# Kernel tuning notes

Measured on AMD Instinct MI355X. Metric: run time of the kernel, lower is better.

The kernel has to match this reference:

```python
import jax, jax.numpy as jnp
import numpy as np

D_MODEL = 768
NUM_HEADS = 12
NUM_REG = 4
EPS = 1e-5


def _layernorm(x, g, b):
    mu = jnp.mean(x, axis=-1, keepdims=True)
    var = jnp.mean(jnp.square(x - mu), axis=-1, keepdims=True)
    return (x - mu) * jax.lax.rsqrt(var + EPS) * g + b


def _make_mask(seq_len):
    # True = masked (disallowed), matching torch attn_mask bool semantics.
    r1 = 1 + NUM_REG
    mask = np.ones((seq_len, seq_len), dtype=bool)
    mask[0, :] = False                      # context token attends to all
    mask[1:r1, :] = False                   # register tokens attend to all
    mask[r1:, :r1] = False                  # (not use_input_context_token) == False
    mask[r1:, r1:] = ~np.eye(seq_len - r1, dtype=bool)  # feature tokens: self only
    return jnp.asarray(mask)


def setup_inputs() -> dict:
    key = jax.random.key(0)
    ks = jax.random.split(key, 16)
    B, C, H, W = 8, D_MODEL, 32, 32
    d = D_MODEL
    s = 0.02
    inp = {
        "x": jax.random.normal(ks[0], (B, C, H, W), jnp.float32),
        "context_token": jax.random.normal(ks[1], (B, 1, d), jnp.float32),
        "register_tokens": jax.random.normal(ks[2], (B, NUM_REG, d), jnp.float32),
        "in_proj_w": jax.random.normal(ks[3], (3 * d, d), jnp.float32) * s,
        "in_proj_b": jnp.zeros((3 * d,), jnp.float32),
        "out_w": jax.random.normal(ks[4], (d, d), jnp.float32) * s,
        "out_b": jnp.zeros((d,), jnp.float32),
        "ln1_g": jnp.ones((d,), jnp.float32),
        "ln1_b": jnp.zeros((d,), jnp.float32),
        "ln2_g": jnp.ones((d,), jnp.float32),
        "ln2_b": jnp.zeros((d,), jnp.float32),
        "w1": jax.random.normal(ks[5], (4 * d, d), jnp.float32) * s,
        "b1": jnp.zeros((4 * d,), jnp.float32),
        "w2": jax.random.normal(ks[6], (d, 4 * d), jnp.float32) * s,
        "b2": jnp.zeros((d,), jnp.float32),
    }
    return inp


def reference(x, context_token, register_tokens, in_proj_w, in_proj_b,
              out_w, out_b, ln1_g, ln1_b, ln2_g, ln2_b, w1, b1, w2, b2):
    B, C, H, W = x.shape
    d, nh = D_MODEL, NUM_HEADS
    hd = d // nh
    x_flat = x.reshape(B, C, H * W).transpose(0, 2, 1)          # [B, HW, d]
    tokens = jnp.concatenate([context_token, register_tokens], axis=1)
    xw = _layernorm(jnp.concatenate([tokens, x_flat], axis=1), ln1_g, ln1_b)  # [B, S, d]
    S = xw.shape[1]

    qkv = xw @ in_proj_w.T + in_proj_b                           # [B, S, 3d]
    q, k, v = jnp.split(qkv, 3, axis=-1)
    q = q.reshape(B, S, nh, hd).transpose(0, 2, 1, 3)            # [B, nh, S, hd]
    k = k.reshape(B, S, nh, hd).transpose(0, 2, 1, 3)
    v = v.reshape(B, S, nh, hd).transpose(0, 2, 1, 3)

    scores = jnp.einsum("bhqd,bhkd->bhqk", q, k) / jnp.sqrt(jnp.float32(hd))
    mask = _make_mask(S)
    scores = jnp.where(mask, jnp.float32(-1e9), scores)
    probs = jax.nn.softmax(scores, axis=-1)
    attn = jnp.einsum("bhqk,bhkd->bhqd", probs, v)               # [B, nh, S, hd]
    attn = attn.transpose(0, 2, 1, 3).reshape(B, S, d)
    attn = attn @ out_w.T + out_b

    h1 = attn + xw                                                # residual
    ff = _layernorm(h1, ln2_g, ln2_b)
    ff = jax.nn.gelu(ff @ w1.T + b1, approximate=False) @ w2.T + b2
    out = ff + h1                                                 # [B, S, d]

    r1 = 1 + NUM_REG
    ctx_out = out[:, 0:1, :]
    reg_out = out[:, 1:r1, :]
    feat_out = out[:, r1:, :].transpose(0, 2, 1).reshape(B, C, H, W)
    return feat_out, ctx_out, reg_out
```

## Files before the change

kernel.cpp:

```cpp
#include <hip/hip_runtime.h>
#include <math.h>
#include <stdint.h>

#define SEQ 1029
#define BATCH 8
#define M_TOT (BATCH * SEQ)
#define M_PAD 8320
#define NCHUNK 17

typedef float floatx4 __attribute__((ext_vector_type(4)));
typedef __bf16 bf16x8 __attribute__((ext_vector_type(8)));

__device__ __forceinline__ unsigned short f2bf(float f) {
  union { float f; unsigned u; } v; v.f = f;
  unsigned r = v.u + 0x7fffu + ((v.u >> 16) & 1u);
  return (unsigned short)(r >> 16);
}
__device__ __forceinline__ float bf2f(unsigned short h) {
  union { unsigned u; float f; } v; v.u = ((unsigned)h) << 16;
  return v.f;
}
__device__ __forceinline__ float bf_lo(unsigned u) { union { unsigned x; float f; } v; v.x = u << 16; return v.f; }
__device__ __forceinline__ float bf_hi(unsigned u) { union { unsigned x; float f; } v; v.x = u & 0xffff0000u; return v.f; }

__device__ __forceinline__ float wave_sum(float v) {
#pragma unroll
  for (int off = 32; off > 0; off >>= 1) v += __shfl_xor(v, off, 64);
  return v;
}
__device__ __forceinline__ float wave_max(float v) {
#pragma unroll
  for (int off = 32; off > 0; off >>= 1) v = fmaxf(v, __shfl_xor(v, off, 64));
  return v;
}

__device__ __forceinline__ void gload16(const unsigned short* g, unsigned short* l) {
  __builtin_amdgcn_global_load_lds(
      (const __attribute__((address_space(1))) unsigned int*)g,
      (__attribute__((address_space(3))) unsigned int*)l, 16, 0, 0);
}

template <int C>
__device__ __forceinline__ void vwait() {
  if constexpr (C == 0) asm volatile("s_waitcnt vmcnt(0)" ::: "memory");
  else if constexpr (C == 4) asm volatile("s_waitcnt vmcnt(4)" ::: "memory");
  else asm volatile("s_waitcnt vmcnt(8)" ::: "memory");
}

#define NQ_QKV 442368
#define NQ_OUT 147456
#define NQ_W1  589824
#define NQ_W2  589824
#define NQ_PAD 8448
__global__ void convert_all(const float4* __restrict__ inw, const float4* __restrict__ outw,
                            const float4* __restrict__ w1, const float4* __restrict__ w2,
                            ushort4* __restrict__ wqkv, ushort4* __restrict__ wout,
                            ushort4* __restrict__ w1b, ushort4* __restrict__ w2b,
                            ushort4* __restrict__ xw_pad, ushort4* __restrict__ attn_pad) {
  const int i = blockIdx.x * 256 + threadIdx.x;
  const float4* src; ushort4* dst; int off;
  if (i < NQ_QKV) { src = inw; dst = wqkv; off = i; }
  else if (i < NQ_QKV + NQ_OUT) { src = outw; dst = wout; off = i - NQ_QKV; }
  else if (i < NQ_QKV + NQ_OUT + NQ_W1) { src = w1; dst = w1b; off = i - NQ_QKV - NQ_OUT; }
  else if (i < NQ_QKV + NQ_OUT + NQ_W1 + NQ_W2) { src = w2; dst = w2b; off = i - NQ_QKV - NQ_OUT - NQ_W1; }
  else {
    const int j = i - (NQ_QKV + NQ_OUT + NQ_W1 + NQ_W2);
    const ushort4 z = {0, 0, 0, 0};
    if (j < NQ_PAD) { xw_pad[j] = z; attn_pad[j] = z; }
    return;
  }
  const float4 v = src[off];
  ushort4 o;
  o.x = f2bf(v.x); o.y = f2bf(v.y); o.z = f2bf(v.z); o.w = f2bf(v.w);
  dst[off] = o;
}
#define NQ_ALL (NQ_QKV + NQ_OUT + NQ_W1 + NQ_W2 + NQ_PAD)

__global__ __launch_bounds__(256) void ln1_feat(const float* __restrict__ x,
                                                const float* __restrict__ g,
                                                const float* __restrict__ bta,
                                                unsigned short* __restrict__ xw) {
  __shared__ float tile[768 * 17];
  const int b = blockIdx.y;
  const int hw0 = blockIdx.x * 16;
  const int t = threadIdx.x;
  const float* xb = x + (size_t)b * 768 * 1024;
  const int cl = t >> 4, hl = t & 15;
  for (int it = 0; it < 48; it++) {
    const int c = it * 16 + cl;
    tile[c * 17 + hl] = xb[(size_t)c * 1024 + hw0 + hl];
  }
  __syncthreads();
  const int wave = t >> 6, lane = t & 63;
  for (int tk = wave; tk < 16; tk += 4) {
    float vals[12], s = 0.f, ss = 0.f;
#pragma unroll
    for (int i = 0; i < 12; i++) {
      const float v = tile[(lane + 64 * i) * 17 + tk];
      vals[i] = v; s += v; ss += v * v;
    }
    s = wave_sum(s); ss = wave_sum(ss);
    const float mu = s * (1.0f / 768.0f);
    const float var = ss * (1.0f / 768.0f) - mu * mu;
    const float rs = rsqrtf(var + 1e-5f);
    const int row = b * SEQ + 5 + hw0 + tk;
    unsigned short* orow = xw + (size_t)row * 768;
#pragma unroll
    for (int i = 0; i < 12; i++) {
      const int c = lane + 64 * i;
      orow[c] = f2bf((vals[i] - mu) * rs * g[c] + bta[c]);
    }
  }
}

__global__ __launch_bounds__(256) void ln1_special(const float* __restrict__ ctx,
                                                   const float* __restrict__ regs,
                                                   const float* __restrict__ g,
                                                   const float* __restrict__ bta,
                                                   unsigned short* __restrict__ xw) {
  const int gw = blockIdx.x * 4 + (threadIdx.x >> 6);
  const int lane = threadIdx.x & 63;
  if (gw >= 40) return;
  const int b = gw / 5, s = gw % 5;
  const float* src = (s == 0) ? (ctx + (size_t)b * 768)
                              : (regs + ((size_t)b * 4 + (s - 1)) * 768);
  float vals[12], sm = 0.f, ss = 0.f;
#pragma unroll
  for (int i = 0; i < 12; i++) {
    const float v = src[lane + 64 * i];
    vals[i] = v; sm += v; ss += v * v;
  }
  sm = wave_sum(sm); ss = wave_sum(ss);
  const float mu = sm * (1.0f / 768.0f);
  const float var = ss * (1.0f / 768.0f) - mu * mu;
  const float rs = rsqrtf(var + 1e-5f);
  unsigned short* orow = xw + (size_t)(b * SEQ + s) * 768;
#pragma unroll
  for (int i = 0; i < 12; i++) {
    const int c = lane + 64 * i;
    orow[c] = f2bf((vals[i] - mu) * rs * g[c] + bta[c]);
  }
}

#define BM 128
#define BN 128
#define BK 32

template <int EPI, int K, int N, int NBUF>
__global__ __launch_bounds__(256, NBUF == 3 ? 3 : 2) void gemm_bt(
    const unsigned short* __restrict__ A,
    const unsigned short* __restrict__ W,
    const float* __restrict__ bias,
    const unsigned short* __restrict__ residb,
    const float* __restrict__ residf,
    float* __restrict__ outf,
    unsigned short* __restrict__ outb) {
  __shared__ alignas(16) unsigned short As[NBUF][BM * BK];
  __shared__ alignas(16) unsigned short Ws[NBUF][BN * BK];
  const int t = threadIdx.x;
  const int wave = t >> 6, lane = t & 63;
  const int quad = lane >> 4, l16 = lane & 15;
  const int wm = (wave & 1) * 64, wn = (wave >> 1) * 64;

  constexpr int GX = N / BN;
  constexpr int NWG = GX * (M_PAD / BM);
  constexpr int Q8 = NWG / 8, R8 = NWG % 8;
  const int flat = blockIdx.y * GX + blockIdx.x;
  const int xcd = flat & 7, idx = flat >> 3;
  const int wgid = (xcd < R8 ? xcd * (Q8 + 1) : R8 * (Q8 + 1) + (xcd - R8) * Q8) + idx;
  const int tileM = (wgid / GX) * BM;
  const int tileN = (wgid % GX) * BN;

  const int rl = lane >> 2;
  const int kc8 = ((lane & 3) ^ ((rl >> 1) & 3)) * 8;
  const unsigned short* Ag = A + (size_t)(tileM + wave * 16 + rl) * K;
  const unsigned short* Wg = W + (size_t)(tileN + wave * 16 + rl) * K;
  const int ldst = wave * 512 + lane * 8;

  const int koff = ((quad ^ ((l16 >> 1) & 3)) * 8);

  const floatx4 zero4 = {0.f, 0.f, 0.f, 0.f};
  floatx4 acc[4][4];
#pragma unroll
  for (int i = 0; i < 4; i++)
#pragma unroll
    for (int j = 0; j < 4; j++) acc[i][j] = zero4;

  auto dma = [&](int k0, int buf) {
    gload16(Ag + k0 + kc8, &As[buf][0] + ldst);
    gload16(Ag + (size_t)64 * K + k0 + kc8, &As[buf][0] + ldst + 2048);
    gload16(Wg + k0 + kc8, &Ws[buf][0] + ldst);
    gload16(Wg + (size_t)64 * K + k0 + kc8, &Ws[buf][0] + ldst + 2048);
  };
  auto compute = [&](int buf) {
    bf16x8 af[4], wf[4];
#pragma unroll
    for (int i = 0; i < 4; i++)
      af[i] = *(const bf16x8*)(&As[buf][0] + (wm + i * 16 + l16) * BK + koff);
#pragma unroll
    for (int j = 0; j < 4; j++)
      wf[j] = *(const bf16x8*)(&Ws[buf][0] + (wn + j * 16 + l16) * BK + koff);
#pragma unroll
    for (int i = 0; i < 4; i++)
#pragma unroll
      for (int j = 0; j < 4; j++)
        acc[i][j] = __builtin_amdgcn_mfma_f32_16x16x32_bf16(af[i], wf[j], acc[i][j], 0, 0, 0);
  };

  constexpr int NSTEP = K / BK;
  constexpr int PF = NBUF - 1;

#pragma unroll
  for (int p = 0; p < PF; ++p) dma(p * BK, p);

  int cb = 0, db = PF % NBUF;
#pragma unroll 1
  for (int i = 0; i < NSTEP - PF; ++i) {
    vwait<4 * (NBUF - 2)>();
    __builtin_amdgcn_s_barrier();
    __builtin_amdgcn_sched_barrier(0);
    dma((i + PF) * BK, db);
    db = (db + 1 == NBUF) ? 0 : db + 1;
    compute(cb);
    cb = (cb + 1 == NBUF) ? 0 : cb + 1;
  }
  if constexpr (NBUF == 4) {
    vwait<8>(); __builtin_amdgcn_s_barrier(); __builtin_amdgcn_sched_barrier(0);
    compute(cb); cb = (cb + 1 == NBUF) ? 0 : cb + 1;
  }
  vwait<4>(); __builtin_amdgcn_s_barrier(); __builtin_amdgcn_sched_barrier(0);
  compute(cb); cb = (cb + 1 == NBUF) ? 0 : cb + 1;
  vwait<0>(); __builtin_amdgcn_s_barrier(); __builtin_amdgcn_sched_barrier(0);
  compute(cb);

#pragma unroll
  for (int i = 0; i < 4; i++) {
    const int mbase = tileM + wm + i * 16 + quad * 4;
#pragma unroll
    for (int j = 0; j < 4; j++) {
      const int n = tileN + wn + j * 16 + l16;
      const float bv = bias[n];
#pragma unroll
      for (int r = 0; r < 4; r++) {
        const size_t idx2 = (size_t)(mbase + r) * N + n;
        float v = acc[i][j][r] + bv;
        if constexpr (EPI == 0) {
          outb[idx2] = f2bf(v);
        } else if constexpr (EPI == 1) {
          outf[idx2] = v + bf2f(residb[idx2]);
        } else if constexpr (EPI == 2) {
          v = 0.5f * v * (1.0f + erff(v * 0.70710678118654752f));
          outb[idx2] = f2bf(v);
        } else {
          outf[idx2] = v + residf[idx2];
        }
      }
    }
  }
}

__global__ __launch_bounds__(256) void attn_feat(const unsigned short* __restrict__ qkv,
                                                 unsigned short* __restrict__ attn) {
  __shared__ float kk[5][64];
  __shared__ float vv[5][64];
  const int b = blockIdx.z, h = blockIdx.y;
  const int t = threadIdx.x;
  const size_t base = (size_t)b * SEQ;
  for (int i = t; i < 320; i += 256) {
    const int j = i >> 6, dd = i & 63;
    const size_t rb = (base + j) * 2304 + (size_t)h * 64 + dd;
    kk[j][dd] = bf2f(qkv[rb + 768]);
    vv[j][dd] = bf2f(qkv[rb + 1536]);
  }
  __syncthreads();
  const int wave = t >> 6, lane = t & 63;
  const int s = 5 + blockIdx.x * 4 + wave;
  const size_t row = (base + s) * 2304 + (size_t)h * 64;
  const float q = bf2f(qkv[row + lane]);
  const float kself = bf2f(qkv[row + 768 + lane]);
  const float vself = bf2f(qkv[row + 1536 + lane]);
  float sc[6];
#pragma unroll
  for (int j = 0; j < 5; j++) sc[j] = wave_sum(q * kk[j][lane]) * 0.125f;
  sc[5] = wave_sum(q * kself) * 0.125f;
  float mx = sc[0];
#pragma unroll
  for (int j = 1; j < 6; j++) mx = fmaxf(mx, sc[j]);
  float den = 0.f, e[6];
#pragma unroll
  for (int j = 0; j < 6; j++) { e[j] = expf(sc[j] - mx); den += e[j]; }
  const float inv = 1.0f / den;
  float o = 0.f;
#pragma unroll
  for (int j = 0; j < 5; j++) o += e[j] * vv[j][lane];
  o += e[5] * vself;
  attn[(base + s) * 768 + (size_t)h * 64 + lane] = f2bf(o * inv);
}

__global__ __launch_bounds__(256) void attn_part(const unsigned short* __restrict__ qkv,
                                                 float* __restrict__ part) {
  __shared__ float qs[5][64];
  __shared__ float sc[5][64];
  __shared__ float mArr[5], lArr[5];
  __shared__ float og[4][320];
  const int c = blockIdx.x, h = blockIdx.y, b = blockIdx.z;
  const int t = threadIdx.x;
  const size_t base = (size_t)b * SEQ;
  const int kbase = (c < 16) ? (5 + 64 * c) : 0;
  const int nvalid = (c < 16) ? 64 : 5;

  for (int i = t; i < 320; i += 256)
    qs[i >> 6][i & 63] = bf2f(qkv[(base + (i >> 6)) * 2304 + (size_t)h * 64 + (i & 63)]);
  __syncthreads();

  const int keyloc = t >> 2, dc = t & 3;
  const int key = kbase + keyloc;
  const unsigned short* krow = qkv + (base + key) * 2304 + 768 + (size_t)h * 64;
  const uint4 k0 = *(const uint4*)(krow + dc * 8);
  const uint4 k1 = *(const uint4*)(krow + dc * 8 + 32);
  float kf[16];
  {
    const unsigned ku[8] = {k0.x, k0.y, k0.z, k0.w, k1.x, k1.y, k1.z, k1.w};
#pragma unroll
    for (int j = 0; j < 8; j++) { kf[2 * j] = bf_lo(ku[j]); kf[2 * j + 1] = bf_hi(ku[j]); }
  }
#pragma unroll
  for (int q = 0; q < 5; q++) {
    const float* qp = qs[q];
    float d0 = 0.f;
#pragma unroll
    for (int j = 0; j < 8; j++) d0 += qp[dc * 8 + j] * kf[j];
#pragma unroll
    for (int j = 0; j < 8; j++) d0 += qp[dc * 8 + 32 + j] * kf[8 + j];
    d0 += __shfl_xor(d0, 1, 64);
    d0 += __shfl_xor(d0, 2, 64);
    if (dc == 0) sc[q][keyloc] = (keyloc < nvalid) ? d0 * 0.125f : -1e30f;
  }
  __syncthreads();

  const int wave = t >> 6, lane = t & 63;
  for (int q = wave; q < 5; q += 4) {
    const float v = sc[q][lane];
    const float m = wave_max(v);
    const float e = expf(v - m);
    sc[q][lane] = e;
    const float l = wave_sum(e);
    if (lane == 0) { mArr[q] = m; lArr[q] = l; }
  }
  __syncthreads();

  const int d = t & 63, g = t >> 6;
  float o[5] = {0.f, 0.f, 0.f, 0.f, 0.f};
  for (int i = 0; i < 16; i++) {
    const int kl = g * 16 + i;
    const float v = bf2f(qkv[(base + kbase + kl) * 2304 + 1536 + (size_t)h * 64 + d]);
#pragma unroll
    for (int q = 0; q < 5; q++) o[q] += sc[q][kl] * v;
  }
#pragma unroll
  for (int q = 0; q < 5; q++) og[g][q * 64 + d] = o[q];
  __syncthreads();

  float* pw = part + (size_t)((b * 12 + h) * NCHUNK + c) * 5 * 66;
  for (int i = t; i < 320; i += 256) {
    const int q = i >> 6, dd = i & 63;
    pw[q * 66 + 2 + dd] = og[0][i] + og[1][i] + og[2][i] + og[3][i];
    if (dd == 0) { pw[q * 66] = mArr[q]; pw[q * 66 + 1] = lArr[q]; }
  }
}

__global__ __launch_bounds__(64) void attn_comb(const float* __restrict__ part,
                                                unsigned short* __restrict__ attn) {
  const int qi = blockIdx.x, h = blockIdx.y, b = blockIdx.z;
  const int d = threadIdx.x;
  float M = -3e38f, L = 0.f, o = 0.f;
  for (int c = 0; c < NCHUNK; c++) {
    const float* p = part + ((size_t)((b * 12 + h) * NCHUNK + c) * 5 + qi) * 66;
    const float mc = p[0], lc = p[1], oc = p[2 + d];
    if (mc > M) {
      const float s = expf(M - mc);
      L = L * s + lc; o = o * s + oc; M = mc;
    } else {
      const float w = expf(mc - M);
      L += lc * w; o += oc * w;
    }
  }
  attn[((size_t)b * SEQ + qi) * 768 + (size_t)h * 64 + d] = f2bf(o / L);
}

__global__ __launch_bounds__(256) void ln2_kernel(const float* __restrict__ h1,
                                                  const float* __restrict__ g,
                                                  const float* __restrict__ bta,
                                                  unsigned short* __restrict__ out) {
  const int row = blockIdx.x * 4 + (threadIdx.x >> 6);
  const int lane = threadIdx.x & 63;
  const float* r = h1 + (size_t)row * 768;
  float vals[12], sm = 0.f, ss = 0.f;
#pragma unroll
  for (int i = 0; i < 12; i++) {
    const float v = r[lane + 64 * i];
    vals[i] = v; sm += v; ss += v * v;
  }
  sm = wave_sum(sm); ss = wave_sum(ss);
  const float mu = sm * (1.0f / 768.0f);
  const float var = ss * (1.0f / 768.0f) - mu * mu;
  const float rs = rsqrtf(var + 1e-5f);
  unsigned short* orow = out + (size_t)row * 768;
#pragma unroll
  for (int i = 0; i < 12; i++) {
    const int c = lane + 64 * i;
    orow[c] = f2bf((vals[i] - mu) * rs * g[c] + bta[c]);
  }
}

__global__ __launch_bounds__(256) void scatter_all(const float* __restrict__ outb,
                                                   float* __restrict__ dout) {
  const int t = threadIdx.x;
  const int b = blockIdx.z;
  if (blockIdx.x == 24) {
    const int i = (b * 32 + blockIdx.y) * 256 + t;
    if (i >= 40 * 768) return;
    const int rowi = i / 768, c = i % 768;
    const int bb = rowi / 5, s = rowi % 5;
    const float v = outb[(size_t)(bb * SEQ + s) * 768 + c];
    if (s == 0) dout[6291456 + (size_t)bb * 768 + c] = v;
    else dout[6291456 + 6144 + ((size_t)bb * 4 + (s - 1)) * 768 + c] = v;
    return;
  }
  __shared__ float tl[32][33];
  const int hw0 = blockIdx.y * 32, c0 = blockIdx.x * 32;
  const int i = t >> 5, j = t & 31;
#pragma unroll
  for (int r = 0; r < 4; r++) {
    const int hwi = i + r * 8;
    tl[hwi][j] = outb[(size_t)(b * SEQ + 5 + hw0 + hwi) * 768 + c0 + j];
  }
  __syncthreads();
#pragma unroll
  for (int r = 0; r < 4; r++) {
    const int ci = i + r * 8;
    dout[(size_t)b * 768 * 1024 + (size_t)(c0 + ci) * 1024 + hw0 + j] = tl[j][ci];
  }
}

extern "C" void kernel_launch(void* const* d_in, const int* in_sizes, int n_in,
                              void* d_out, int out_size, void* d_ws, size_t ws_size,
                              hipStream_t stream) {
  const float* x    = (const float*)d_in[0];
  const float* ctx  = (const float*)d_in[1];
  const float* regs = (const float*)d_in[2];
  const float* inw  = (const float*)d_in[3];
  const float* inb  = (const float*)d_in[4];
  const float* outw = (const float*)d_in[5];
  const float* outbi= (const float*)d_in[6];
  const float* ln1g = (const float*)d_in[7];
  const float* ln1b = (const float*)d_in[8];
  const float* ln2g = (const float*)d_in[9];
  const float* ln2b = (const float*)d_in[10];
  const float* w1   = (const float*)d_in[11];
  const float* b1   = (const float*)d_in[12];
  const float* w2   = (const float*)d_in[13];
  const float* b2   = (const float*)d_in[14];

  char* ws = (char*)d_ws;
  unsigned short* wqkv_b = (unsigned short*)(ws + 0);
  unsigned short* wout_b = (unsigned short*)(ws + 3538944);
  unsigned short* w1_b   = (unsigned short*)(ws + 4718592);
  unsigned short* w2_b   = (unsigned short*)(ws + 9437184);
  unsigned short* xw_b   = (unsigned short*)(ws + 14155776);
  unsigned short* ln2o_b = (unsigned short*)(ws + 26935296);
  float*          h1_f   = (float*)(ws + 39714816);
  unsigned short* qkv_b  = (unsigned short*)(ws + 65273856);
  unsigned short* attn_b = (unsigned short*)(ws + 103612416);
  float*          out_f  = (float*)(ws + 14155776);
  unsigned short* ffm_b  = (unsigned short*)(ws + 65273856);
  float*          part_f = (float*)(ws + 39714816);
  float* dout = (float*)d_out;

  convert_all<<<(NQ_ALL + 255) / 256, 256, 0, stream>>>(
      (const float4*)inw, (const float4*)outw, (const float4*)w1, (const float4*)w2,
      (ushort4*)wqkv_b, (ushort4*)wout_b, (ushort4*)w1_b, (ushort4*)w2_b,
      (ushort4*)(xw_b + (size_t)M_TOT * 768), (ushort4*)(attn_b + (size_t)M_TOT * 768));

  ln1_feat<<<dim3(64, 8), 256, 0, stream>>>(x, ln1g, ln1b, xw_b);
  ln1_special<<<10, 256, 0, stream>>>(ctx, regs, ln1g, ln1b, xw_b);

  gemm_bt<0, 768, 2304, 3><<<dim3(2304 / BN, M_PAD / BM), 256, 0, stream>>>(
      xw_b, wqkv_b, inb, nullptr, nullptr, nullptr, qkv_b);

  attn_feat<<<dim3(256, 12, 8), 256, 0, stream>>>(qkv_b, attn_b);
  attn_part<<<dim3(NCHUNK, 12, 8), 256, 0, stream>>>(qkv_b, part_f);
  attn_comb<<<dim3(5, 12, 8), 64, 0, stream>>>(part_f, attn_b);

  gemm_bt<1, 768, 768, 4><<<dim3(768 / BN, M_PAD / BM), 256, 0, stream>>>(
      attn_b, wout_b, outbi, xw_b, nullptr, h1_f, nullptr);

  ln2_kernel<<<M_PAD / 4, 256, 0, stream>>>(h1_f, ln2g, ln2b, ln2o_b);

  gemm_bt<2, 768, 3072, 3><<<dim3(3072 / BN, M_PAD / BM), 256, 0, stream>>>(
      ln2o_b, w1_b, b1, nullptr, nullptr, nullptr, ffm_b);

  gemm_bt<3, 3072, 768, 4><<<dim3(768 / BN, M_PAD / BM), 256, 0, stream>>>(
      ffm_b, w2_b, b2, nullptr, h1_f, out_f, nullptr);

  scatter_all<<<dim3(25, 32, 8), 256, 0, stream>>>(out_f, dout);
}
```

Baseline: 419.6 us.

## Add 256x256-tile XCD-swizzled GEMM for FFN1 and polynomial GELU

The FFN up-projection now uses a new 512-thread GEMM kernel with 256x256 tiles, a 4-buffer direct-to-LDS prefetch pipeline and an XCD-aware workgroup remap. The larger tile is meant to raise data reuse per LDS load and improve L2 locality for this large GEMM. Exact erff in the GELU epilogue is also replaced by an Abramowitz-Stegun polynomial using a fast reciprocal and exp. Risks: the M tiling does not divide M_PAD (8320/256), so the last tile row reads A past the padded rows, and the large LDS footprint limits occupancy.

```diff
diff --git a/kernel.cpp b/kernel.cpp
--- a/kernel.cpp
+++ b/kernel.cpp
@@ -32,6 +32,15 @@
 #pragma unroll
   for (int off = 32; off > 0; off >>= 1) v = fmaxf(v, __shfl_xor(v, off, 64));
   return v;
+}
+
+__device__ __forceinline__ float fast_gelu(float v) {
+  const float ax = fabsf(v) * 0.70710678118654752f;
+  const float t = __builtin_amdgcn_rcpf(1.0f + 0.3275911f * ax);
+  const float poly = ((((1.061405429f * t - 1.453152027f) * t + 1.421413741f) * t
+                       - 0.284496736f) * t + 0.254829592f) * t;
+  const float er = 1.0f - poly * __expf(-ax * ax);
+  return 0.5f * v * (1.0f + copysignf(er, v));
 }
 
 __device__ __forceinline__ void gload16(const unsigned short* g, unsigned short* l) {
@@ -249,10 +258,114 @@
         } else if constexpr (EPI == 1) {
           outf[idx2] = v + bf2f(residb[idx2]);
         } else if constexpr (EPI == 2) {
-          v = 0.5f * v * (1.0f + erff(v * 0.70710678118654752f));
-          outb[idx2] = f2bf(v);
+          outb[idx2] = f2bf(fast_gelu(v));
         } else {
           outf[idx2] = v + residf[idx2];
+        }
+      }
+    }
+  }
+}
+
+#define BM2 256
+#define BN2 256
+
+template <int EPI, int K, int N>
+__global__ __launch_bounds__(512, 2) void gemm_big(
+    const unsigned short* __restrict__ A,
+    const unsigned short* __restrict__ W,
+    const float* __restrict__ bias,
+    unsigned short* __restrict__ outb) {
+  __shared__ alignas(16) unsigned short As[4][BM2 * BK];
+  __shared__ alignas(16) unsigned short Ws[4][BN2 * BK];
+  const int t = threadIdx.x;
+  const int wave = t >> 6, lane = t & 63;
+  const int quad = lane >> 4, l16 = lane & 15;
+  const int wm = (wave & 1) * 128, wn = (wave >> 1) * 64;
+
+  constexpr int GX = N / BN2;
+  constexpr int GY = (M_PAD + BM2 - 1) / BM2;
+  constexpr int NWG = GX * GY;
+  constexpr int Q8 = NWG / 8, R8 = NWG % 8;
+  const int flat = blockIdx.y * GX + blockIdx.x;
+  const int xcd = flat & 7, idx = flat >> 3;
+  const int wgid = (xcd < R8 ? xcd * (Q8 + 1) : R8 * (Q8 + 1) + (xcd - R8) * Q8) + idx;
+  const int tileM = (wgid / GX) * BM2;
+  const int tileN = (wgid % GX) * BN2;
+
+  const int rl = lane >> 2;
+  const int kc8 = ((lane & 3) ^ ((rl >> 1) & 3)) * 8;
+  const unsigned short* Ag = A + (size_t)(tileM + wave * 16 + rl) * K;
+  const unsigned short* Wg = W + (size_t)(tileN + wave * 16 + rl) * K;
+  const int ldst = wave * 512 + lane * 8;
+
+  const int koff = ((quad ^ ((l16 >> 1) & 3)) * 8);
+
+  const floatx4 zero4 = {0.f, 0.f, 0.f, 0.f};
+  floatx4 acc[8][4];
+#pragma unroll
+  for (int i = 0; i < 8; i++)
+#pragma unroll
+    for (int j = 0; j < 4; j++) acc[i][j] = zero4;
+
+  auto dma = [&](int k0, int buf) {
+    gload16(Ag + k0 + kc8, &As[buf][0] + ldst);
+    gload16(Ag + (size_t)128 * K + k0 + kc8, &As[buf][0] + ldst + 4096);
+    gload16(Wg + k0 + kc8, &Ws[buf][0] + ldst);
+    gload16(Wg + (size_t)128 * K + k0 + kc8, &Ws[buf][0] + ldst + 4096);
+  };
+  auto compute = [&](int buf) {
+    bf16x8 af[8], wf[4];
+#pragma unroll
+    for (int i = 0; i < 8; i++)
+      af[i] = *(const bf16x8*)(&As[buf][0] + (wm + i * 16 + l16) * BK + koff);
+#pragma unroll
+    for (int j = 0; j < 4; j++)
+      wf[j] = *(const bf16x8*)(&Ws[buf][0] + (wn + j * 16 + l16) * BK + koff);
+#pragma unroll
+    for (int i = 0; i < 8; i++)
+#pragma unroll
+      for (int j = 0; j < 4; j++)
+        acc[i][j] = __builtin_amdgcn_mfma_f32_16x16x32_bf16(af[i], wf[j], acc[i][j], 0, 0, 0);
+  };
+
+  constexpr int NSTEP = K / BK;
+  constexpr int PF = 3;
+
+  dma(0, 0); dma(BK, 1); dma(2 * BK, 2);
+
+  int cb = 0, db = 3;
+#pragma unroll 1
+  for (int i = 0; i < NSTEP - PF; ++i) {
+    vwait<8>();
+    __builtin_amdgcn_s_barrier();
+    __builtin_amdgcn_sched_barrier(0);
+    dma((i + PF) * BK, db);
+    db = (db + 1) & 3;
+    compute(cb);
+    cb = (cb + 1) & 3;
+  }
+  vwait<8>(); __builtin_amdgcn_s_barrier(); __builtin_amdgcn_sched_barrier(0);
+  compute(cb); cb = (cb + 1) & 3;
+  vwait<4>(); __builtin_amdgcn_s_barrier(); __builtin_amdgcn_sched_barrier(0);
+  compute(cb); cb = (cb + 1) & 3;
+  vwait<0>(); __builtin_amdgcn_s_barrier(); __builtin_amdgcn_sched_barrier(0);
+  compute(cb);
+
+#pragma unroll
+  for (int i = 0; i < 8; i++) {
+    const int mbase = tileM + wm + i * 16 + quad * 4;
+#pragma unroll
+    for (int j = 0; j < 4; j++) {
+      const int n = tileN + wn + j * 16 + l16;
+      const float bv = bias[n];
+#pragma unroll
+      for (int r = 0; r < 4; r++) {
+        if (mbase + r < M_PAD) {
+          const size_t idx2 = (size_t)(mbase + r) * N + n;
+          float v = acc[i][j][r] + bv;
+          if constexpr (EPI == 2) v = fast_gelu(v);
+          outb[idx2] = f2bf(v);
         }
       }
     }
@@ -497,8 +610,8 @@
 
   ln2_kernel<<<M_PAD / 4, 256, 0, stream>>>(h1_f, ln2g, ln2b, ln2o_b);
 
-  gemm_bt<2, 768, 3072, 3><<<dim3(3072 / BN, M_PAD / BM), 256, 0, stream>>>(
-      ln2o_b, w1_b, b1, nullptr, nullptr, nullptr, ffm_b);
+  gemm_big<2, 768, 3072><<<dim3(3072 / BN2, (M_PAD + BM2 - 1) / BM2), 512, 0, stream>>>(
+      ln2o_b, w1_b, b1, ffm_b);
 
   gemm_bt<3, 3072, 768, 4><<<dim3(768 / BN, M_PAD / BM), 256, 0, stream>>>(
       ffm_b, w2_b, b2, nullptr, h1_f, out_f, nullptr);
```

New measurement: 435.9 us. 1.04x slower.
